# Optimization experiments

Hardware: AMD Instinct MI355X
Metric: run time of the kernel (lower is better)

Reference implementation:

```python
import jax, jax.numpy as jnp
import numpy as np

B, T, J, C = 32, 256, 21, 3
BT = B * T
N = BT * J

_TPL_SRC = np.array([0, 1, 2, 3, 4, 0, 5, 6, 7, 8, 0, 9, 10, 11, 12, 0, 13, 14, 15, 16, 0, 17, 18, 19, 20], np.int32)
_TPL_DST = np.array([1, 2, 3, 4, 0, 5, 6, 7, 8, 0, 9, 10, 11, 12, 0, 13, 14, 15, 16, 0, 17, 18, 19, 20, 0], np.int32)


def _build_edges():
    off = (np.arange(BT, dtype=np.int32) * J)[:, None]
    src = (_TPL_SRC[None, :] + off).ravel()
    dst = (_TPL_DST[None, :] + off).ravel()
    # PyG GATConv default add_self_loops=True (both layers see the same augmented set)
    loops = np.arange(N, dtype=np.int32)
    return np.concatenate([src, loops]), np.concatenate([dst, loops])


def setup_inputs() -> dict:
    key = jax.random.key(0)
    ks = jax.random.split(key, 8)
    src, dst = _build_edges()
    return {
        "keypoints": jax.random.normal(ks[0], (B, T, J, C), jnp.float32),
        "W1": jax.random.normal(ks[1], (3, 256), jnp.float32) * 0.3,
        "att1_src": jax.random.normal(ks[2], (4, 64), jnp.float32) * 0.1,
        "att1_dst": jax.random.normal(ks[3], (4, 64), jnp.float32) * 0.1,
        "b1": jnp.zeros((256,), jnp.float32),
        "W2": jax.random.normal(ks[4], (256, 128), jnp.float32) * 0.06,
        "att2_src": jax.random.normal(ks[5], (1, 128), jnp.float32) * 0.1,
        "att2_dst": jax.random.normal(ks[6], (1, 128), jnp.float32) * 0.1,
        "b2": jnp.zeros((128,), jnp.float32),
        "src": jnp.asarray(src),
        "dst": jnp.asarray(dst),
    }


def _gat_conv(x, src, dst, W, a_src, a_dst, b, heads, d_head):
    n = x.shape[0]
    h = (x @ W).reshape(n, heads, d_head)            # [N,H,D]
    e_s = jnp.einsum('nhd,hd->nh', h, a_src)          # [N,H]
    e_d = jnp.einsum('nhd,hd->nh', h, a_dst)
    e = jax.nn.leaky_relu(e_s[src] + e_d[dst], 0.2)   # [E,H]
    m = jax.ops.segment_max(e, dst, num_segments=n)
    ex = jnp.exp(e - m[dst])
    z = jax.ops.segment_sum(ex, dst, num_segments=n)
    alpha = ex / z[dst]                               # scatter-softmax over dst
    out = jax.ops.segment_sum(h[src] * alpha[:, :, None], dst, num_segments=n)
    return out.reshape(n, heads * d_head) + b


def reference(keypoints, W1, att1_src, att1_dst, b1, W2, att2_src, att2_dst, b2, src, dst):
    x = keypoints.reshape(N, C)
    x = jax.nn.relu(_gat_conv(x, src, dst, W1, att1_src, att1_dst, b1, 4, 64))
    x = jax.nn.relu(_gat_conv(x, src, dst, W2, att2_src, att2_dst, b2, 1, 128))
    x = x.reshape(BT, J, 128).mean(axis=1)            # pool joints
    return x.reshape(B, T, 128).mean(axis=1)          # pool time -> [B,128]
```

## Files before the change

### kernel.cpp

```cpp
#include <hip/hip_runtime.h>

#define NJ  21
#define X1S 264
#define H2S 136
#define XAS 40

typedef __attribute__((ext_vector_type(8))) short  bf16x8;
typedef __attribute__((ext_vector_type(4))) float  floatx4;

__device__ __forceinline__ float lrelu(float v){ return v > 0.f ? v : 0.2f*v; }
__device__ __forceinline__ unsigned short f2bf(float x){
  unsigned int u = __float_as_uint(x);
  return (unsigned short)((u + 0x7FFFu + ((u >> 16) & 1u)) >> 16);
}
__device__ __forceinline__ float bf2f(unsigned short h){
  return __uint_as_float(((unsigned int)h) << 16);
}

__global__ void prep(const float* __restrict__ W1, const float* __restrict__ a1s,
                     const float* __restrict__ a1d, const float* __restrict__ W2,
                     unsigned short* __restrict__ w2f, unsigned short* __restrict__ w1b,
                     float* __restrict__ ws1o, float* __restrict__ out){
  const int t = threadIdx.x, b = blockIdx.x;
  if (b < 32){
    int base = b*1024 + t*4;
    #pragma unroll
    for (int i = 0; i < 4; ++i){
      int idx = base + i;
      int j = idx & 7, lane = (idx >> 3) & 63, nt = (idx >> 9) & 7, kt = idx >> 12;
      int k = kt*32 + (lane >> 4)*8 + j;
      int n = nt*16 + (lane & 15);
      w2f[idx] = f2bf(W2[k*128 + n]);
    }
  } else if (b < 40){
    int base = (b - 32)*1024 + t*4;
    #pragma unroll
    for (int i = 0; i < 4; ++i){
      int idx = base + i;
      int j = idx & 7, lane = (idx >> 3) & 63, nt = idx >> 9;
      int k = (lane >> 4)*8 + j;
      int n = nt*16 + (lane & 15);
      float v = 0.f;
      if (k < 16){
        int h = k >> 2, c = k & 3;
        if (c < 3 && h == (n >> 6)) v = W1[c*256 + n];
      }
      w1b[idx] = f2bf(v);
    }
  } else {
    if (t < 24){
      int c = t % 3, h = (t/3) & 3, sd = t/12;
      const float* av = sd ? a1d : a1s;
      float s = 0.f;
      #pragma unroll
      for (int d = 0; d < 64; ++d) s += W1[c*256 + h*64 + d]*av[h*64 + d];
      ws1o[sd*12 + c*4 + h] = s;
    }
    for (int i = t; i < 4096; i += 256) out[i] = 0.f;
  }
}

__global__ __launch_bounds__(256, 5)
void gat_fused(const float* __restrict__ kp,  const float* __restrict__ b1v,
               const float* __restrict__ a2s, const float* __restrict__ a2d,
               const float* __restrict__ b2v, const unsigned short* __restrict__ w2f,
               const unsigned short* __restrict__ w1b, const float* __restrict__ ws1g,
               float* __restrict__ out)
{
  __shared__ float xsL[2][NJ][4];
  __shared__ unsigned char uni[3840] __attribute__((aligned(16)));
  __shared__ unsigned short x1bf[48*X1S];
  __shared__ float a2sL[128], a2dL[128];
  unsigned short* xagb  = (unsigned short*)uni;
  float*          es2   = (float*)uni;
  float*          ed2   = (float*)(uni + 176);
  float (*al2L)[8]      = (float(*)[8])(uni + 352);
  float*          pool2 = (float*)(uni + 1792);
  unsigned short* h2bf  = x1bf;

  const int t = threadIdx.x, blk = blockIdx.x;
  const int w = t >> 6, lane = t & 63, quad = lane >> 4, ln15 = lane & 15;
  const int h = t & 3;

  float wsr[3], wdr[3];
  #pragma unroll
  for (int c = 0; c < 3; ++c){ wsr[c] = ws1g[c*4 + h]; wdr[c] = ws1g[12 + c*4 + h]; }

  if (t < 126){ int fl = t >= 63; int r = t - 63*fl; xsL[fl][r/3][r%3] = kp[blk*126 + t]; }
  if (t < 128) a2sL[t] = a2s[t]; else a2dL[t-128] = a2d[t-128];
  for (int o = t; o < 960; o += 256) ((unsigned*)xagb)[o] = 0u;
  __syncthreads();

  if (t < 168){
    int fn = t >> 2, fl = fn >= NJ, n = fn - fl*NJ;
    int p[6], np;
    if (n == 0){ p[0]=4;p[1]=8;p[2]=12;p[3]=16;p[4]=20;p[5]=0; np=6; }
    else       { p[0]=(n%4==1)?0:(n-1); p[1]=n; np=2; }
    float4 xself = *(const float4*)&xsL[fl][n][0];
    float ed = xself.x*wdr[0] + xself.y*wdr[1] + xself.z*wdr[2];
    float4 xp[6]; float e[6]; float m = -1e30f;
    for (int i = 0; i < np; ++i){
      xp[i] = *(const float4*)&xsL[fl][p[i]][0];
      float es = xp[i].x*wsr[0] + xp[i].y*wsr[1] + xp[i].z*wsr[2];
      e[i] = lrelu(es + ed); m = fmaxf(m, e[i]);
    }
    float z = 0.f;
    for (int i = 0; i < np; ++i){ e[i] = __expf(e[i]-m); z += e[i]; }
    float inv = 1.f/z;
    float a0 = 0.f, a1 = 0.f, a2v = 0.f;
    for (int i = 0; i < np; ++i){
      float al = e[i]*inv;
      a0 += al*xp[i].x; a1 += al*xp[i].y; a2v += al*xp[i].z;
    }
    uint2 pk;
    pk.x = (unsigned)f2bf(a0) | ((unsigned)f2bf(a1) << 16);
    pk.y = (unsigned)f2bf(a2v);
    *(uint2*)&xagb[fn*XAS + h*4] = pk;
  }
  __syncthreads();

  {
    bf16x8 A0 = *(bf16x8*)&xagb[(     ln15)*XAS + quad*8];
    bf16x8 A1 = *(bf16x8*)&xagb[(16 + ln15)*XAS + quad*8];
    bf16x8 A2 = *(bf16x8*)&xagb[(32 + ln15)*XAS + quad*8];
    #pragma unroll
    for (int i = 0; i < 4; ++i){
      const int cb = w*64 + i*16 + ln15;
      bf16x8 Bv = *(const bf16x8*)(w1b + (unsigned)((w*4 + i)*64 + lane)*8);
      floatx4 c0 = {0.f,0.f,0.f,0.f}, c1 = c0, c2 = c0;
      c0 = __builtin_amdgcn_mfma_f32_16x16x32_bf16(A0, Bv, c0, 0,0,0);
      c1 = __builtin_amdgcn_mfma_f32_16x16x32_bf16(A1, Bv, c1, 0,0,0);
      c2 = __builtin_amdgcn_mfma_f32_16x16x32_bf16(A2, Bv, c2, 0,0,0);
      float bb = b1v[cb];
      #pragma unroll
      for (int r = 0; r < 4; ++r){
        x1bf[(     quad*4 + r)*X1S + cb] = f2bf(fmaxf(c0[r] + bb, 0.f));
        x1bf[(16 + quad*4 + r)*X1S + cb] = f2bf(fmaxf(c1[r] + bb, 0.f));
        x1bf[(32 + quad*4 + r)*X1S + cb] = f2bf(fmaxf(c2[r] + bb, 0.f));
      }
    }
  }
  __syncthreads();

  floatx4 acc[3][2];
  #pragma unroll
  for (int mt = 0; mt < 3; ++mt){ acc[mt][0] = (floatx4){0.f,0.f,0.f,0.f}; acc[mt][1] = acc[mt][0]; }
  #pragma unroll
  for (int kt = 0; kt < 8; ++kt){
    bf16x8 a0 = *(bf16x8*)&x1bf[(     ln15)*X1S + kt*32 + quad*8];
    bf16x8 a1 = *(bf16x8*)&x1bf[(16 + ln15)*X1S + kt*32 + quad*8];
    bf16x8 a2 = *(bf16x8*)&x1bf[(32 + ln15)*X1S + kt*32 + quad*8];
    bf16x8 b0 = *(const bf16x8*)(w2f + (unsigned)((kt*8 + 2*w    )*64 + lane)*8);
    bf16x8 b1 = *(const bf16x8*)(w2f + (unsigned)((kt*8 + 2*w + 1)*64 + lane)*8);
    acc[0][0] = __builtin_amdgcn_mfma_f32_16x16x32_bf16(a0, b0, acc[0][0], 0,0,0);
    acc[0][1] = __builtin_amdgcn_mfma_f32_16x16x32_bf16(a0, b1, acc[0][1], 0,0,0);
    acc[1][0] = __builtin_amdgcn_mfma_f32_16x16x32_bf16(a1, b0, acc[1][0], 0,0,0);
    acc[1][1] = __builtin_amdgcn_mfma_f32_16x16x32_bf16(a1, b1, acc[1][1], 0,0,0);
    acc[2][0] = __builtin_amdgcn_mfma_f32_16x16x32_bf16(a2, b0, acc[2][0], 0,0,0);
    acc[2][1] = __builtin_amdgcn_mfma_f32_16x16x32_bf16(a2, b1, acc[2][1], 0,0,0);
  }
  __syncthreads();
  {
    const int c0 = 32*w + ln15, c1 = c0 + 16;
    #pragma unroll
    for (int mt = 0; mt < 3; ++mt){
      #pragma unroll
      for (int r = 0; r < 4; ++r){
        int row = mt*16 + quad*4 + r;
        if (row < 42){
          h2bf[row*H2S + c0] = f2bf(acc[mt][0][r]);
          h2bf[row*H2S + c1] = f2bf(acc[mt][1][r]);
        }
      }
    }
  }
  __syncthreads();

  if (t < 168){
    int fn = t >> 2, q = t & 3;
    float s = 0.f, d = 0.f;
    #pragma unroll
    for (int jb = 0; jb < 4; ++jb){
      bf16x8 hv = *(bf16x8*)&h2bf[fn*H2S + q*32 + jb*8];
      float4 as0 = *(const float4*)&a2sL[q*32 + jb*8];
      float4 as1 = *(const float4*)&a2sL[q*32 + jb*8 + 4];
      float4 ad0 = *(const float4*)&a2dL[q*32 + jb*8];
      float4 ad1 = *(const float4*)&a2dL[q*32 + jb*8 + 4];
      float h0 = bf2f((unsigned short)hv[0]), h1 = bf2f((unsigned short)hv[1]);
      float h2v= bf2f((unsigned short)hv[2]), h3 = bf2f((unsigned short)hv[3]);
      float h4 = bf2f((unsigned short)hv[4]), h5 = bf2f((unsigned short)hv[5]);
      float h6 = bf2f((unsigned short)hv[6]), h7 = bf2f((unsigned short)hv[7]);
      s += h0*as0.x + h1*as0.y + h2v*as0.z + h3*as0.w
         + h4*as1.x + h5*as1.y + h6*as1.z  + h7*as1.w;
      d += h0*ad0.x + h1*ad0.y + h2v*ad0.z + h3*ad0.w
         + h4*ad1.x + h5*ad1.y + h6*ad1.z  + h7*ad1.w;
    }
    s += __shfl_xor(s, 1); s += __shfl_xor(s, 2);
    d += __shfl_xor(d, 1); d += __shfl_xor(d, 2);
    if (q == 0){ es2[fn] = s; ed2[fn] = d; }
  }
  __syncthreads();

  if (t < 42){
    int fl = t >= NJ, n = t - fl*NJ, base = fl*NJ;
    int p[6], np;
    if (n == 0){ p[0]=4;p[1]=8;p[2]=12;p[3]=16;p[4]=20;p[5]=0; np=6; }
    else       { p[0]=(n%4==1)?0:(n-1); p[1]=n; np=2; }
    float ed = ed2[t];
    float e[6], m = -1e30f;
    for (int i = 0; i < np; ++i){ e[i] = lrelu(es2[base + p[i]] + ed); m = fmaxf(m, e[i]); }
    float z = 0.f;
    for (int i = 0; i < np; ++i){ e[i] = __expf(e[i]-m); z += e[i]; }
    float inv = 1.f/z;
    for (int i = 0; i < np; ++i) al2L[t][i] = e[i]*inv;
  }
  __syncthreads();

  {
    int fl = t >> 7, j = t & 127, base = fl*NJ;
    float bj = b2v[j];
    float h0 = bf2f(h2bf[base*H2S + j]);
    float v0 = al2L[base][5]*h0;
    float s = 0.f, hprev = h0;
    #pragma unroll
    for (int n = 1; n < NJ; ++n){
      float hn = bf2f(h2bf[(base+n)*H2S + j]);
      float pv = ((n & 3) == 1) ? h0 : hprev;
      float2 al = *(const float2*)&al2L[base+n][0];
      s += fmaxf(bj + al.x*pv + al.y*hn, 0.f);
      if ((n & 3) == 0) v0 += al2L[base][(n >> 2) - 1]*hn;
      hprev = hn;
    }
    s += fmaxf(bj + v0, 0.f);
    if (t >= 128) pool2[j] = s;
    __syncthreads();
    if (t < 128) atomicAdd(&out[(blk >> 7)*128 + j], (s + pool2[j])*(1.f/5376.f));
  }
}

extern "C" void kernel_launch(void* const* d_in, const int* in_sizes, int n_in,
                              void* d_out, int out_size, void* d_ws, size_t ws_size,
                              hipStream_t stream){
  const float* kp  = (const float*)d_in[0];
  const float* W1  = (const float*)d_in[1];
  const float* a1s = (const float*)d_in[2];
  const float* a1d = (const float*)d_in[3];
  const float* b1  = (const float*)d_in[4];
  const float* W2  = (const float*)d_in[5];
  const float* a2s = (const float*)d_in[6];
  const float* a2d = (const float*)d_in[7];
  const float* b2  = (const float*)d_in[8];
  float* out = (float*)d_out;

  unsigned short* w2f = (unsigned short*)d_ws;
  unsigned short* w1b = (unsigned short*)((char*)d_ws + 65536);
  float* ws1 = (float*)((char*)d_ws + 65536 + 16384);

  prep<<<41, 256, 0, stream>>>(W1, a1s, a1d, W2, w2f, w1b, ws1, out);
  gat_fused<<<4096, 256, 0, stream>>>(kp, b1, a2s, a2d, b2, w2f, w1b, ws1, out);
}
```

Measured before the change: 129.0 us.

## Restructure GAT layer-2 epilogue per wave, keep h2 in fp32, prefetch GEMM operands

The layer-2 attention scores, the softmax and the aggregation now each run inside a single wave per frame. Those stages use wave-local fences instead of three block-wide barriers, and the h2 features stay in LDS as fp32 rather than being rounded back to bf16. The layer-2 MFMA loop is software-pipelined with register double-buffering of the A tiles and a three-deep rotation of the W2 fragments. Layer-1 weight and bias loads are hoisted ahead of the MFMAs, and the bf16 rounding uses a cheaper round-half-up. Two smaller changes: the xagb zero-fill is folded into the aggregation writes, and the h2 row stride changes to 132 floats. In exchange, only two waves do the epilogue, global atomics per block double, and correctness relies on lockstep visibility of LDS within a wave.

```diff
diff --git a/kernel.cpp b/kernel.cpp
--- a/kernel.cpp
+++ b/kernel.cpp
@@ -2,7 +2,7 @@
 
 #define NJ  21
 #define X1S 264
-#define H2S 136
+#define H2S 132
 #define XAS 40
 
 typedef __attribute__((ext_vector_type(8))) short  bf16x8;
@@ -13,8 +13,8 @@
   unsigned int u = __float_as_uint(x);
   return (unsigned short)((u + 0x7FFFu + ((u >> 16) & 1u)) >> 16);
 }
-__device__ __forceinline__ float bf2f(unsigned short h){
-  return __uint_as_float(((unsigned int)h) << 16);
+__device__ __forceinline__ unsigned short f2bf_u(float x){
+  return (unsigned short)((__float_as_uint(x) + 0x8000u) >> 16);
 }
 
 __global__ void prep(const float* __restrict__ W1, const float* __restrict__ a1s,
@@ -68,31 +68,27 @@
                float* __restrict__ out)
 {
   __shared__ float xsL[2][NJ][4];
-  __shared__ unsigned char uni[3840] __attribute__((aligned(16)));
-  __shared__ unsigned short x1bf[48*X1S];
+  __shared__ unsigned short xagb[48*XAS] __attribute__((aligned(16)));
   __shared__ float a2sL[128], a2dL[128];
-  unsigned short* xagb  = (unsigned short*)uni;
-  float*          es2   = (float*)uni;
-  float*          ed2   = (float*)(uni + 176);
-  float (*al2L)[8]      = (float(*)[8])(uni + 352);
-  float*          pool2 = (float*)(uni + 1792);
-  unsigned short* h2bf  = x1bf;
+  __shared__ unsigned short x1bf[48*X1S] __attribute__((aligned(16)));
+  float* h2f = (float*)x1bf;
+  float* esL = (float*)xagb;
+  float* edL = (float*)((char*)xagb + 176);
+  float (*al2F)[NJ][8] = (float(*)[NJ][8])((char*)xagb + 352);
 
   const int t = threadIdx.x, blk = blockIdx.x;
   const int w = t >> 6, lane = t & 63, quad = lane >> 4, ln15 = lane & 15;
   const int h = t & 3;
 
-  float wsr[3], wdr[3];
-  #pragma unroll
-  for (int c = 0; c < 3; ++c){ wsr[c] = ws1g[c*4 + h]; wdr[c] = ws1g[12 + c*4 + h]; }
-
   if (t < 126){ int fl = t >= 63; int r = t - 63*fl; xsL[fl][r/3][r%3] = kp[blk*126 + t]; }
   if (t < 128) a2sL[t] = a2s[t]; else a2dL[t-128] = a2d[t-128];
-  for (int o = t; o < 960; o += 256) ((unsigned*)xagb)[o] = 0u;
   __syncthreads();
 
   if (t < 168){
     int fn = t >> 2, fl = fn >= NJ, n = fn - fl*NJ;
+    float wsr[3], wdr[3];
+    #pragma unroll
+    for (int c = 0; c < 3; ++c){ wsr[c] = ws1g[c*4 + h]; wdr[c] = ws1g[12 + c*4 + h]; }
     int p[6], np;
     if (n == 0){ p[0]=4;p[1]=8;p[2]=12;p[3]=16;p[4]=20;p[5]=0; np=6; }
     else       { p[0]=(n%4==1)?0:(n-1); p[1]=n; np=2; }
@@ -116,6 +112,8 @@
     pk.x = (unsigned)f2bf(a0) | ((unsigned)f2bf(a1) << 16);
     pk.y = (unsigned)f2bf(a2v);
     *(uint2*)&xagb[fn*XAS + h*4] = pk;
+    uint2 z2; z2.x = 0u; z2.y = 0u;
+    *(uint2*)&xagb[fn*XAS + 16 + h*4] = z2;
   }
   __syncthreads();
 
@@ -123,20 +121,24 @@
     bf16x8 A0 = *(bf16x8*)&xagb[(     ln15)*XAS + quad*8];
     bf16x8 A1 = *(bf16x8*)&xagb[(16 + ln15)*XAS + quad*8];
     bf16x8 A2 = *(bf16x8*)&xagb[(32 + ln15)*XAS + quad*8];
+    bf16x8 Bv[4]; float bb[4];
+    #pragma unroll
+    for (int i = 0; i < 4; ++i){
+      Bv[i] = *(const bf16x8*)(w1b + (unsigned)((w*4 + i)*64 + lane)*8);
+      bb[i] = b1v[w*64 + i*16 + ln15];
+    }
     #pragma unroll
     for (int i = 0; i < 4; ++i){
       const int cb = w*64 + i*16 + ln15;
-      bf16x8 Bv = *(const bf16x8*)(w1b + (unsigned)((w*4 + i)*64 + lane)*8);
       floatx4 c0 = {0.f,0.f,0.f,0.f}, c1 = c0, c2 = c0;
-      c0 = __builtin_amdgcn_mfma_f32_16x16x32_bf16(A0, Bv, c0, 0,0,0);
-      c1 = __builtin_amdgcn_mfma_f32_16x16x32_bf16(A1, Bv, c1, 0,0,0);
-      c2 = __builtin_amdgcn_mfma_f32_16x16x32_bf16(A2, Bv, c2, 0,0,0);
-      float bb = b1v[cb];
+      c0 = __builtin_amdgcn_mfma_f32_16x16x32_bf16(A0, Bv[i], c0, 0,0,0);
+      c1 = __builtin_amdgcn_mfma_f32_16x16x32_bf16(A1, Bv[i], c1, 0,0,0);
+      c2 = __builtin_amdgcn_mfma_f32_16x16x32_bf16(A2, Bv[i], c2, 0,0,0);
       #pragma unroll
       for (int r = 0; r < 4; ++r){
-        x1bf[(     quad*4 + r)*X1S + cb] = f2bf(fmaxf(c0[r] + bb, 0.f));
-        x1bf[(16 + quad*4 + r)*X1S + cb] = f2bf(fmaxf(c1[r] + bb, 0.f));
-        x1bf[(32 + quad*4 + r)*X1S + cb] = f2bf(fmaxf(c2[r] + bb, 0.f));
+        x1bf[(     quad*4 + r)*X1S + cb] = f2bf_u(fmaxf(c0[r] + bb[i], 0.f));
+        x1bf[(16 + quad*4 + r)*X1S + cb] = f2bf_u(fmaxf(c1[r] + bb[i], 0.f));
+        x1bf[(32 + quad*4 + r)*X1S + cb] = f2bf_u(fmaxf(c2[r] + bb[i], 0.f));
       }
     }
   }
@@ -145,19 +147,29 @@
   floatx4 acc[3][2];
   #pragma unroll
   for (int mt = 0; mt < 3; ++mt){ acc[mt][0] = (floatx4){0.f,0.f,0.f,0.f}; acc[mt][1] = acc[mt][0]; }
-  #pragma unroll
-  for (int kt = 0; kt < 8; ++kt){
-    bf16x8 a0 = *(bf16x8*)&x1bf[(     ln15)*X1S + kt*32 + quad*8];
-    bf16x8 a1 = *(bf16x8*)&x1bf[(16 + ln15)*X1S + kt*32 + quad*8];
-    bf16x8 a2 = *(bf16x8*)&x1bf[(32 + ln15)*X1S + kt*32 + quad*8];
-    bf16x8 b0 = *(const bf16x8*)(w2f + (unsigned)((kt*8 + 2*w    )*64 + lane)*8);
-    bf16x8 b1 = *(const bf16x8*)(w2f + (unsigned)((kt*8 + 2*w + 1)*64 + lane)*8);
-    acc[0][0] = __builtin_amdgcn_mfma_f32_16x16x32_bf16(a0, b0, acc[0][0], 0,0,0);
-    acc[0][1] = __builtin_amdgcn_mfma_f32_16x16x32_bf16(a0, b1, acc[0][1], 0,0,0);
-    acc[1][0] = __builtin_amdgcn_mfma_f32_16x16x32_bf16(a1, b0, acc[1][0], 0,0,0);
-    acc[1][1] = __builtin_amdgcn_mfma_f32_16x16x32_bf16(a1, b1, acc[1][1], 0,0,0);
-    acc[2][0] = __builtin_amdgcn_mfma_f32_16x16x32_bf16(a2, b0, acc[2][0], 0,0,0);
-    acc[2][1] = __builtin_amdgcn_mfma_f32_16x16x32_bf16(a2, b1, acc[2][1], 0,0,0);
+  {
+    #define LDA(row0, kt) (*(bf16x8*)&x1bf[((row0) + ln15)*X1S + (kt)*32 + quad*8])
+    #define LDB(kt, half) (*(const bf16x8*)(w2f + (unsigned)(((kt)*8 + 2*w + (half))*64 + lane)*8))
+    bf16x8 A0c = LDA(0,0), A1c = LDA(16,0), A2c = LDA(32,0);
+    bf16x8 B0s[3], B1s[3];
+    #pragma unroll
+    for (int i = 0; i < 3; ++i){ B0s[i] = LDB(i,0); B1s[i] = LDB(i,1); }
+    #pragma unroll
+    for (int kt = 0; kt < 8; ++kt){
+      bf16x8 b0c = B0s[kt%3], b1c = B1s[kt%3];
+      bf16x8 A0n, A1n, A2n;
+      if (kt < 7){ A0n = LDA(0,kt+1); A1n = LDA(16,kt+1); A2n = LDA(32,kt+1); }
+      if (kt < 5){ B0s[kt%3] = LDB(kt+3,0); B1s[kt%3] = LDB(kt+3,1); }
+      acc[0][0] = __builtin_amdgcn_mfma_f32_16x16x32_bf16(A0c, b0c, acc[0][0], 0,0,0);
+      acc[0][1] = __builtin_amdgcn_mfma_f32_16x16x32_bf16(A0c, b1c, acc[0][1], 0,0,0);
+      acc[1][0] = __builtin_amdgcn_mfma_f32_16x16x32_bf16(A1c, b0c, acc[1][0], 0,0,0);
+      acc[1][1] = __builtin_amdgcn_mfma_f32_16x16x32_bf16(A1c, b1c, acc[1][1], 0,0,0);
+      acc[2][0] = __builtin_amdgcn_mfma_f32_16x16x32_bf16(A2c, b0c, acc[2][0], 0,0,0);
+      acc[2][1] = __builtin_amdgcn_mfma_f32_16x16x32_bf16(A2c, b1c, acc[2][1], 0,0,0);
+      if (kt < 7){ A0c = A0n; A1c = A1n; A2c = A2n; }
+    }
+    #undef LDA
+    #undef LDB
   }
   __syncthreads();
   {
@@ -168,73 +180,67 @@
       for (int r = 0; r < 4; ++r){
         int row = mt*16 + quad*4 + r;
         if (row < 42){
-          h2bf[row*H2S + c0] = f2bf(acc[mt][0][r]);
-          h2bf[row*H2S + c1] = f2bf(acc[mt][1][r]);
+          h2f[row*H2S + c0] = acc[mt][0][r];
+          h2f[row*H2S + c1] = acc[mt][1][r];
         }
       }
     }
   }
   __syncthreads();
 
-  if (t < 168){
-    int fn = t >> 2, q = t & 3;
+  if (w < 2){
+    const int fl = w;
     float s = 0.f, d = 0.f;
-    #pragma unroll
-    for (int jb = 0; jb < 4; ++jb){
-      bf16x8 hv = *(bf16x8*)&h2bf[fn*H2S + q*32 + jb*8];
-      float4 as0 = *(const float4*)&a2sL[q*32 + jb*8];
-      float4 as1 = *(const float4*)&a2sL[q*32 + jb*8 + 4];
-      float4 ad0 = *(const float4*)&a2dL[q*32 + jb*8];
-      float4 ad1 = *(const float4*)&a2dL[q*32 + jb*8 + 4];
-      float h0 = bf2f((unsigned short)hv[0]), h1 = bf2f((unsigned short)hv[1]);
-      float h2v= bf2f((unsigned short)hv[2]), h3 = bf2f((unsigned short)hv[3]);
-      float h4 = bf2f((unsigned short)hv[4]), h5 = bf2f((unsigned short)hv[5]);
-      float h6 = bf2f((unsigned short)hv[6]), h7 = bf2f((unsigned short)hv[7]);
-      s += h0*as0.x + h1*as0.y + h2v*as0.z + h3*as0.w
-         + h4*as1.x + h5*as1.y + h6*as1.z  + h7*as1.w;
-      d += h0*ad0.x + h1*ad0.y + h2v*ad0.z + h3*ad0.w
-         + h4*ad1.x + h5*ad1.y + h6*ad1.z  + h7*ad1.w;
-    }
-    s += __shfl_xor(s, 1); s += __shfl_xor(s, 2);
-    d += __shfl_xor(d, 1); d += __shfl_xor(d, 2);
-    if (q == 0){ es2[fn] = s; ed2[fn] = d; }
-  }
-  __syncthreads();
-
-  if (t < 42){
-    int fl = t >= NJ, n = t - fl*NJ, base = fl*NJ;
-    int p[6], np;
-    if (n == 0){ p[0]=4;p[1]=8;p[2]=12;p[3]=16;p[4]=20;p[5]=0; np=6; }
-    else       { p[0]=(n%4==1)?0:(n-1); p[1]=n; np=2; }
-    float ed = ed2[t];
-    float e[6], m = -1e30f;
-    for (int i = 0; i < np; ++i){ e[i] = lrelu(es2[base + p[i]] + ed); m = fmaxf(m, e[i]); }
-    float z = 0.f;
-    for (int i = 0; i < np; ++i){ e[i] = __expf(e[i]-m); z += e[i]; }
-    float inv = 1.f/z;
-    for (int i = 0; i < np; ++i) al2L[t][i] = e[i]*inv;
-  }
-  __syncthreads();
-
-  {
-    int fl = t >> 7, j = t & 127, base = fl*NJ;
-    float bj = b2v[j];
-    float h0 = bf2f(h2bf[base*H2S + j]);
-    float v0 = al2L[base][5]*h0;
-    float s = 0.f, hprev = h0;
-    #pragma unroll
-    for (int n = 1; n < NJ; ++n){
-      float hn = bf2f(h2bf[(base+n)*H2S + j]);
-      float pv = ((n & 3) == 1) ? h0 : hprev;
-      float2 al = *(const float2*)&al2L[base+n][0];
-      s += fmaxf(bj + al.x*pv + al.y*hn, 0.f);
-      if ((n & 3) == 0) v0 += al2L[base][(n >> 2) - 1]*hn;
-      hprev = hn;
-    }
-    s += fmaxf(bj + v0, 0.f);
-    if (t >= 128) pool2[j] = s;
-    __syncthreads();
-    if (t < 128) atomicAdd(&out[(blk >> 7)*128 + j], (s + pool2[j])*(1.f/5376.f));
+    if (lane < 42){
+      int n = lane >> 1, cb2 = (lane & 1)*64;
+      const float* hp  = h2f + (fl*NJ + n)*H2S + cb2;
+      const float* asp = a2sL + cb2;
+      const float* adp = a2dL + cb2;
+      #pragma unroll
+      for (int c = 0; c < 64; c += 4){
+        float4 hv = *(const float4*)(hp + c);
+        float4 av = *(const float4*)(asp + c);
+        float4 dv = *(const float4*)(adp + c);
+        s += hv.x*av.x + hv.y*av.y + hv.z*av.z + hv.w*av.w;
+        d += hv.x*dv.x + hv.y*dv.y + hv.z*dv.z + hv.w*dv.w;
+      }
+    }
+    s += __shfl_xor(s, 1); d += __shfl_xor(d, 1);
+    if (lane < 42 && (lane & 1) == 0){ esL[fl*NJ + (lane>>1)] = s; edL[fl*NJ + (lane>>1)] = d; }
+    __threadfence_block();
+    if (lane < NJ){
+      int n = lane;
+      int p[6], np;
+      if (n == 0){ p[0]=4;p[1]=8;p[2]=12;p[3]=16;p[4]=20;p[5]=0; np=6; }
+      else       { p[0]=(n%4==1)?0:(n-1); p[1]=n; np=2; }
+      float ed = edL[fl*NJ + n];
+      float e[6], m = -1e30f;
+      for (int i = 0; i < np; ++i){ e[i] = lrelu(esL[fl*NJ + p[i]] + ed); m = fmaxf(m, e[i]); }
+      float z = 0.f;
+      for (int i = 0; i < np; ++i){ e[i] = __expf(e[i]-m); z += e[i]; }
+      float inv = 1.f/z;
+      for (int i = 0; i < np; ++i) al2F[fl][n][i] = e[i]*inv;
+    }
+    __threadfence_block();
+    #pragma unroll
+    for (int jj = 0; jj < 2; ++jj){
+      int j = lane + jj*64;
+      float bj = b2v[j];
+      float h0 = h2f[(fl*NJ)*H2S + j];
+      float v0 = al2F[fl][0][5]*h0;
+      float sum = 0.f, hprev = h0;
+      #pragma unroll
+      for (int n = 1; n < NJ; ++n){
+        float hn = h2f[(fl*NJ + n)*H2S + j];
+        float pv = ((n & 3) == 1) ? h0 : hprev;
+        float2 al = *(const float2*)&al2F[fl][n][0];
+        sum += fmaxf(bj + al.x*pv + al.y*hn, 0.f);
+        if ((n & 3) == 0) v0 += al2F[fl][0][(n >> 2) - 1]*hn;
+        hprev = hn;
+      }
+      sum += fmaxf(bj + v0, 0.f);
+      atomicAdd(&out[(blk >> 7)*128 + j], sum*(1.f/5376.f));
+    }
   }
 }
 
```

Result: slower. 139.9 us (+8.5%).
